# Performance work log

Measured on AMD Instinct MI355X. Metric: run time of the kernel, lower is better.

## Reference

```python
import jax, jax.numpy as jnp
import numpy as np

EPS = 1e-8  # torch.cosine_similarity default eps

def setup_inputs() -> dict:
    key = jax.random.key(0)
    k1, k2, k3 = jax.random.split(key, 3)
    N, D = 65536, 512
    tensor_1 = jax.random.normal(k1, (N, D), dtype=jnp.float32)
    tensor_2 = jax.random.normal(k2, (N, D), dtype=jnp.float32)
    labels = jax.random.randint(k3, (N,), 0, 3, dtype=jnp.int64)
    return {"tensor_1": tensor_1, "tensor_2": tensor_2, "labels": labels, "device": 0}

def reference(tensor_1, tensor_2, labels, device):
    # tag == 'mci_ol': labels in {0,2} -> accumulate (1 - cos), else -> |cos|;
    # divide total by tensor_1.shape[0]. NOTE: original indexes rows by the
    # LABEL VALUE (tensor_1[idx]), which we preserve.
    a = tensor_1[labels]            # [B, D] gathered by label value
    b = tensor_2[labels]            # [B, D]
    dot = jnp.sum(a * b, axis=-1)   # [B]
    na = jnp.sqrt(jnp.sum(a * a, axis=-1))
    nb = jnp.sqrt(jnp.sum(b * b, axis=-1))
    cos = dot / jnp.maximum(na * nb, EPS)
    mask1 = (labels == 2) | (labels == 0)
    total = jnp.sum(jnp.where(mask1, 1.0 - cos, jnp.abs(cos)))
    loss = total / tensor_1.shape[0]
    return loss.reshape(1)
```

## Files before the change

kernel.cpp:

```cpp
#include <hip/hip_runtime.h>

#define D 512
#define EPS 1e-8f

__global__ __launch_bounds__(256) void OrthogonalLoss_kernel(
    const float* __restrict__ t1, const float* __restrict__ t2,
    const int* __restrict__ labels, float* __restrict__ out,
    unsigned int* __restrict__ ws, int n, int nblocks)
{
    unsigned int* counts = ws;
    unsigned int* ticket = ws + 3;
    float* cosv = (float*)(ws + 4);

    const int tid = threadIdx.x;
    const int gid = blockIdx.x * blockDim.x + tid;

    int n0 = 0, n1 = 0, n2 = 0;
    const int4* lab4 = (const int4*)labels;
    if (gid * 4 < n) {
        int4 v = lab4[gid];
        n0 = (v.x == 0) + (v.y == 0) + (v.z == 0) + (v.w == 0);
        n1 = (v.x == 1) + (v.y == 1) + (v.z == 1) + (v.w == 1);
        n2 = (v.x == 2) + (v.y == 2) + (v.z == 2) + (v.w == 2);
    }

    #pragma unroll
    for (int off = 32; off >= 1; off >>= 1) {
        n0 += __shfl_down(n0, off);
        n1 += __shfl_down(n1, off);
        n2 += __shfl_down(n2, off);
    }
    if ((tid & 63) == 0) {
        atomicAdd(&counts[0], (unsigned)n0);
        atomicAdd(&counts[1], (unsigned)n1);
        atomicAdd(&counts[2], (unsigned)n2);
    }

    if (blockIdx.x == 0) {
        float dot[3] = {0.f, 0.f, 0.f};
        float na[3]  = {0.f, 0.f, 0.f};
        float nb[3]  = {0.f, 0.f, 0.f};
        for (int d = tid; d < D; d += 256) {
            #pragma unroll
            for (int l = 0; l < 3; ++l) {
                float a = t1[l * D + d];
                float b = t2[l * D + d];
                dot[l] += a * b;
                na[l]  += a * a;
                nb[l]  += b * b;
            }
        }
        #pragma unroll
        for (int off = 32; off >= 1; off >>= 1) {
            #pragma unroll
            for (int l = 0; l < 3; ++l) {
                dot[l] += __shfl_down(dot[l], off);
                na[l]  += __shfl_down(na[l], off);
                nb[l]  += __shfl_down(nb[l], off);
            }
        }
        __shared__ float red[4][9];
        const int wave = tid >> 6;
        if ((tid & 63) == 0) {
            #pragma unroll
            for (int l = 0; l < 3; ++l) {
                red[wave][l * 3 + 0] = dot[l];
                red[wave][l * 3 + 1] = na[l];
                red[wave][l * 3 + 2] = nb[l];
            }
        }
        __syncthreads();
        if (tid == 0) {
            #pragma unroll
            for (int l = 0; l < 3; ++l) {
                float dd = 0.f, aa = 0.f, bb = 0.f;
                #pragma unroll
                for (int w = 0; w < 4; ++w) {
                    dd += red[w][l * 3 + 0];
                    aa += red[w][l * 3 + 1];
                    bb += red[w][l * 3 + 2];
                }
                float c = dd / fmaxf(sqrtf(aa) * sqrtf(bb), EPS);
                atomicAdd(&cosv[l], c);
            }
        }
    }

    __syncthreads();
    __threadfence();
    if (tid == 0) {
        unsigned old = atomicAdd(ticket, 1u);
        if (old == (unsigned)(nblocks - 1)) {
            float c0 = atomicAdd(&cosv[0], 0.0f);
            float c1 = atomicAdd(&cosv[1], 0.0f);
            float c2 = atomicAdd(&cosv[2], 0.0f);
            unsigned m0 = atomicAdd(&counts[0], 0u);
            unsigned m1 = atomicAdd(&counts[1], 0u);
            unsigned m2 = atomicAdd(&counts[2], 0u);
            float total = (float)m0 * (1.0f - c0)
                        + (float)m2 * (1.0f - c2)
                        + (float)m1 * fabsf(c1);
            out[0] = total / (float)n;
        }
    }
}

extern "C" void kernel_launch(void* const* d_in, const int* in_sizes, int n_in,
                              void* d_out, int out_size, void* d_ws, size_t ws_size,
                              hipStream_t stream) {
    const float* t1     = (const float*)d_in[0];
    const float* t2     = (const float*)d_in[1];
    const int*   labels = (const int*)d_in[2];
    float* out = (float*)d_out;

    const int n = in_sizes[2];
    const int nthreads = (n + 3) / 4;
    const int nblocks = (nthreads + 255) / 256;

    hipMemsetAsync(d_ws, 0, 64, stream);
    OrthogonalLoss_kernel<<<nblocks, 256, 0, stream>>>(
        t1, t2, labels, out, (unsigned int*)d_ws, n, nblocks);
}
```

Baseline: 225.1 us.

## Collapse multi-block atomic reduction into a single 1024-thread block

```diff
diff --git a/kernel.cpp b/kernel.cpp
--- a/kernel.cpp
+++ b/kernel.cpp
@@ -1,107 +1,82 @@
 #include <hip/hip_runtime.h>
 
-#define D 512
 #define EPS 1e-8f
 
-__global__ __launch_bounds__(256) void OrthogonalLoss_kernel(
+__global__ __launch_bounds__(1024) void OrthogonalLoss_kernel(
     const float* __restrict__ t1, const float* __restrict__ t2,
-    const int* __restrict__ labels, float* __restrict__ out,
-    unsigned int* __restrict__ ws, int n, int nblocks)
+    const int* __restrict__ labels, float* __restrict__ out, int n)
 {
-    unsigned int* counts = ws;
-    unsigned int* ticket = ws + 3;
-    float* cosv = (float*)(ws + 4);
+    const int tid  = threadIdx.x;
+    const int wave = tid >> 6;
 
-    const int tid = threadIdx.x;
-    const int gid = blockIdx.x * blockDim.x + tid;
+    __shared__ int   redc[16][2];
+    __shared__ float redf[8][9];
 
-    int n0 = 0, n1 = 0, n2 = 0;
+    int c0 = 0, c1 = 0;
+    const int n4 = n >> 2;
     const int4* lab4 = (const int4*)labels;
-    if (gid * 4 < n) {
-        int4 v = lab4[gid];
-        n0 = (v.x == 0) + (v.y == 0) + (v.z == 0) + (v.w == 0);
-        n1 = (v.x == 1) + (v.y == 1) + (v.z == 1) + (v.w == 1);
-        n2 = (v.x == 2) + (v.y == 2) + (v.z == 2) + (v.w == 2);
+    for (int i = tid; i < n4; i += 1024) {
+        int4 v = lab4[i];
+        c0 += (v.x == 0) + (v.y == 0) + (v.z == 0) + (v.w == 0);
+        c1 += (v.x == 1) + (v.y == 1) + (v.z == 1) + (v.w == 1);
     }
-
+    for (int i = (n4 << 2) + tid; i < n; i += 1024) {
+        int v = labels[i];
+        c0 += (v == 0);
+        c1 += (v == 1);
+    }
     #pragma unroll
     for (int off = 32; off >= 1; off >>= 1) {
-        n0 += __shfl_down(n0, off);
-        n1 += __shfl_down(n1, off);
-        n2 += __shfl_down(n2, off);
+        c0 += __shfl_down(c0, off);
+        c1 += __shfl_down(c1, off);
     }
-    if ((tid & 63) == 0) {
-        atomicAdd(&counts[0], (unsigned)n0);
-        atomicAdd(&counts[1], (unsigned)n1);
-        atomicAdd(&counts[2], (unsigned)n2);
+    if ((tid & 63) == 0) { redc[wave][0] = c0; redc[wave][1] = c1; }
+
+    float vals[9];
+    if (tid < 512) {
+        float a0 = t1[tid], a1 = t1[512 + tid], a2 = t1[1024 + tid];
+        float b0 = t2[tid], b1 = t2[512 + tid], b2 = t2[1024 + tid];
+        vals[0] = a0 * b0; vals[1] = a0 * a0; vals[2] = b0 * b0;
+        vals[3] = a1 * b1; vals[4] = a1 * a1; vals[5] = b1 * b1;
+        vals[6] = a2 * b2; vals[7] = a2 * a2; vals[8] = b2 * b2;
+    } else {
+        #pragma unroll
+        for (int j = 0; j < 9; ++j) vals[j] = 0.f;
     }
-
-    if (blockIdx.x == 0) {
-        float dot[3] = {0.f, 0.f, 0.f};
-        float na[3]  = {0.f, 0.f, 0.f};
-        float nb[3]  = {0.f, 0.f, 0.f};
-        for (int d = tid; d < D; d += 256) {
-            #pragma unroll
-            for (int l = 0; l < 3; ++l) {
-                float a = t1[l * D + d];
-                float b = t2[l * D + d];
-                dot[l] += a * b;
-                na[l]  += a * a;
-                nb[l]  += b * b;
-            }
-        }
+    #pragma unroll
+    for (int off = 32; off >= 1; off >>= 1) {
         #pragma unroll
-        for (int off = 32; off >= 1; off >>= 1) {
-            #pragma unroll
-            for (int l = 0; l < 3; ++l) {
-                dot[l] += __shfl_down(dot[l], off);
-                na[l]  += __shfl_down(na[l], off);
-                nb[l]  += __shfl_down(nb[l], off);
-            }
-        }
-        __shared__ float red[4][9];
-        const int wave = tid >> 6;
-        if ((tid & 63) == 0) {
-            #pragma unroll
-            for (int l = 0; l < 3; ++l) {
-                red[wave][l * 3 + 0] = dot[l];
-                red[wave][l * 3 + 1] = na[l];
-                red[wave][l * 3 + 2] = nb[l];
-            }
-        }
-        __syncthreads();
-        if (tid == 0) {
-            #pragma unroll
-            for (int l = 0; l < 3; ++l) {
-                float dd = 0.f, aa = 0.f, bb = 0.f;
-                #pragma unroll
-                for (int w = 0; w < 4; ++w) {
-                    dd += red[w][l * 3 + 0];
-                    aa += red[w][l * 3 + 1];
-                    bb += red[w][l * 3 + 2];
-                }
-                float c = dd / fmaxf(sqrtf(aa) * sqrtf(bb), EPS);
-                atomicAdd(&cosv[l], c);
-            }
-        }
+        for (int j = 0; j < 9; ++j) vals[j] += __shfl_down(vals[j], off);
+    }
+    if (tid < 512 && (tid & 63) == 0) {
+        #pragma unroll
+        for (int j = 0; j < 9; ++j) redf[wave][j] = vals[j];
     }
 
     __syncthreads();
-    __threadfence();
+
     if (tid == 0) {
-        unsigned old = atomicAdd(ticket, 1u);
-        if (old == (unsigned)(nblocks - 1)) {
-            float c0 = atomicAdd(&cosv[0], 0.0f);
-            float c1 = atomicAdd(&cosv[1], 0.0f);
-            float c2 = atomicAdd(&cosv[2], 0.0f);
-            unsigned m0 = atomicAdd(&counts[0], 0u);
-            unsigned m1 = atomicAdd(&counts[1], 0u);
-            unsigned m2 = atomicAdd(&counts[2], 0u);
-            float total = (float)m0 * (1.0f - c0)
-                        + (float)m2 * (1.0f - c2)
-                        + (float)m1 * fabsf(c1);
-            out[0] = total / (float)n;
+        int n0 = 0, n1 = 0;
+        #pragma unroll
+        for (int w = 0; w < 16; ++w) { n0 += redc[w][0]; n1 += redc[w][1]; }
+        int n2 = n - n0 - n1;
+
+        float s[9];
+        #pragma unroll
+        for (int j = 0; j < 9; ++j) {
+            float t = 0.f;
+            #pragma unroll
+            for (int w = 0; w < 8; ++w) t += redf[w][j];
+            s[j] = t;
         }
+        float cos0 = s[0] / fmaxf(sqrtf(s[1]) * sqrtf(s[2]), EPS);
+        float cos1 = s[3] / fmaxf(sqrtf(s[4]) * sqrtf(s[5]), EPS);
+        float cos2 = s[6] / fmaxf(sqrtf(s[7]) * sqrtf(s[8]), EPS);
+
+        float total = (float)n0 * (1.0f - cos0)
+                    + (float)n2 * (1.0f - cos2)
+                    + (float)n1 * fabsf(cos1);
+        out[0] = total / (float)n;
     }
 }
 
@@ -114,10 +89,5 @@
     float* out = (float*)d_out;
 
     const int n = in_sizes[2];
-    const int nthreads = (n + 3) / 4;
-    const int nblocks = (nthreads + 255) / 256;
-
-    hipMemsetAsync(d_ws, 0, 64, stream);
-    OrthogonalLoss_kernel<<<nblocks, 256, 0, stream>>>(
-        t1, t2, labels, out, (unsigned int*)d_ws, n, nblocks);
+    OrthogonalLoss_kernel<<<1, 1024, 0, stream>>>(t1, t2, labels, out, n);
 }
```

Result: faster. 219.0 us (-2.7%).
